# Optimization experiments

Hardware: AMD Instinct MI355X
Metric: run time of the kernel (lower is better)

## Reference

```python
import jax, jax.numpy as jnp
import numpy as np

DIM, BIN = 128, 16
LN_EPS = 1e-5


def setup_inputs() -> dict:
    key = jax.random.key(0)
    ks = jax.random.split(key, 16)
    B, Ld, Lc, O = 4096, 50, 50, 64
    D_VOCAB, C_VOCAB = 100000, 1000
    inp = {
        "discrete_index": jax.random.randint(ks[0], (B, Ld), 0, D_VOCAB, dtype=jnp.int32),
        "discrete_mask": jax.random.randint(ks[1], (B, Ld), 0, 2, dtype=jnp.int32),
        "continue_value": jax.random.normal(ks[2], (B, Lc), dtype=jnp.float32),
        "continue_index": jax.random.randint(ks[3], (B, Lc), 0, C_VOCAB, dtype=jnp.int32),
        "continue_mask": jax.random.randint(ks[4], (B, Lc), 0, 2, dtype=jnp.int32),
        # learned parameters (last row = padding idx, zeroed like torch padding_idx init semantics)
        "disc_emb": jax.random.normal(ks[5], (D_VOCAB + 1, DIM), dtype=jnp.float32).at[D_VOCAB].set(0.0),
        "v_emb": jax.random.normal(ks[6], (C_VOCAB + 1, BIN), dtype=jnp.float32).at[C_VOCAB].set(0.0),
        "b1_emb": jax.random.normal(ks[7], (C_VOCAB + 1, BIN), dtype=jnp.float32).at[C_VOCAB].set(0.0),
        "w_emb": jax.random.normal(ks[8], (C_VOCAB + 1, DIM * BIN), dtype=jnp.float32).at[C_VOCAB].set(0.0),
        "b2_emb": jax.random.normal(ks[9], (C_VOCAB + 1, DIM), dtype=jnp.float32).at[C_VOCAB].set(0.0),
        "ln_gamma": jnp.ones((BIN,), dtype=jnp.float32),
        "ln_beta": jnp.zeros((BIN,), dtype=jnp.float32),
        "transform_matrix": jax.random.normal(ks[10], (O, Ld + Lc), dtype=jnp.float32),
    }
    return inp


def reference(discrete_index, discrete_mask, continue_value, continue_index, continue_mask,
              disc_emb, v_emb, b1_emb, w_emb, b2_emb, ln_gamma, ln_beta, transform_matrix):
    B, Lc = continue_index.shape
    # embedding gathers
    discrete_part = disc_emb[discrete_index]            # [B, Ld, D]
    v = v_emb[continue_index]                           # [B, Lc, BIN]
    b1 = b1_emb[continue_index]                         # [B, Lc, BIN]
    w = w_emb[continue_index].reshape(B, Lc, BIN, DIM)  # [B, Lc, BIN, D]
    b2 = b2_emb[continue_index]                         # [B, Lc, D]
    # per-token mini-MLP: LayerNorm(bin) + ReLU + bmm with per-token weight
    h = continue_value[..., None] * v + b1              # [B, Lc, BIN]
    mu = jnp.mean(h, axis=-1, keepdims=True)
    var = jnp.mean((h - mu) ** 2, axis=-1, keepdims=True)
    hn = (h - mu) * jax.lax.rsqrt(var + LN_EPS) * ln_gamma + ln_beta
    a = jax.nn.relu(hn)
    continuous_part = jnp.einsum('blk,blkd->bld', a, w) + b2  # [B, Lc, D]
    parts = jnp.concatenate([discrete_part, continuous_part], axis=1)  # [B, L, D]
    out = jnp.einsum('ol,bld->bod', transform_matrix, parts)           # [B, O, D]
    # mask (no-grad path in original)
    mvec = jnp.concatenate([1 - discrete_mask, 1 - continue_mask], axis=1).astype(jnp.float32)  # [B, L]
    full_mask = (1.0 - jnp.sign(jnp.einsum('ol,bl->bo', transform_matrix, mvec))).astype(jnp.int32)  # [B, O]
    return out, full_mask
```

## Files before the change

### kernel.cpp

```cpp
#include <hip/hip_runtime.h>
#include <hip/hip_bf16.h>

#define NB 4096
#define LD_ 50
#define LC_ 50
#define LTOT 100
#define DIM 128
#define BIN 16
#define NO 64
#define KPAD 128
#define LP 136
#define LN_EPS 1e-5f

typedef __attribute__((ext_vector_type(8))) short bf16x8;
typedef __attribute__((ext_vector_type(4))) float f32x4;

__device__ __forceinline__ unsigned short f2bf(float f) {
    return __builtin_bit_cast(unsigned short, __float2bfloat16(f));
}

__global__ __launch_bounds__(256) void convT_kernel(const float* __restrict__ T,
                                                    unsigned short* __restrict__ Tbf) {
    int t = blockIdx.x * 256 + threadIdx.x;
    if (t < NO * KPAD) {
        int o = t >> 7, k = t & 127;
        float v = (k < LTOT) ? T[o * LTOT + k] : 0.f;
        Tbf[t] = f2bf(v);
    }
}

__global__ __launch_bounds__(256) void fused_embed_kernel(
    const int* __restrict__ dindex,
    const int* __restrict__ dmask,
    const float* __restrict__ cval,
    const int* __restrict__ cindex,
    const int* __restrict__ cmask,
    const float* __restrict__ disc_emb,
    const float* __restrict__ v_emb,
    const float* __restrict__ b1_emb,
    const float* __restrict__ w_emb,
    const float* __restrict__ b2_emb,
    const float* __restrict__ ln_gamma,
    const float* __restrict__ ln_beta,
    const float* __restrict__ T,
    const unsigned short* __restrict__ Tbf,
    float* __restrict__ out,
    float* __restrict__ outmask)
{
    __shared__ unsigned short PbfT[DIM * LP];
    __shared__ float a_lds[LC_ * 17];
    __shared__ float buf32[8 * DIM];
    __shared__ float mvec[LTOT];

    const int b   = blockIdx.x;
    const int tid = threadIdx.x;

    if (tid < LC_) {
        const int l = tid;
        const int ci = cindex[b * LC_ + l];
        const float cv = cval[b * LC_ + l];
        float h[BIN];
        {
            const float4* V4  = reinterpret_cast<const float4*>(v_emb  + (size_t)ci * BIN);
            const float4* B14 = reinterpret_cast<const float4*>(b1_emb + (size_t)ci * BIN);
            #pragma unroll
            for (int q = 0; q < 4; ++q) {
                float4 vv = V4[q], b1v = B14[q];
                h[q*4+0] = cv * vv.x + b1v.x;
                h[q*4+1] = cv * vv.y + b1v.y;
                h[q*4+2] = cv * vv.z + b1v.z;
                h[q*4+3] = cv * vv.w + b1v.w;
            }
        }
        float mu = 0.f;
        #pragma unroll
        for (int k = 0; k < BIN; ++k) mu += h[k];
        mu *= (1.f / BIN);
        float var = 0.f;
        #pragma unroll
        for (int k = 0; k < BIN; ++k) { float t = h[k] - mu; var += t * t; }
        var *= (1.f / BIN);
        const float rstd = rsqrtf(var + LN_EPS);
        #pragma unroll
        for (int k = 0; k < BIN; ++k) {
            float a = (h[k] - mu) * rstd * ln_gamma[k] + ln_beta[k];
            a_lds[l * 17 + k] = fmaxf(a, 0.f);
        }
    }

    if (tid < LTOT) {
        int m = (tid < LD_) ? dmask[b * LD_ + tid] : cmask[b * LC_ + (tid - LD_)];
        mvec[tid] = 1.0f - (float)m;
    }

    {
        const int d  = tid & 127;
        const int hh = tid >> 7;
        unsigned short* row = &PbfT[d * LP];
        if (hh == 0) {
            #pragma unroll
            for (int q = 0; q < 4; ++q)
                *reinterpret_cast<uint2*>(&row[100 + q * 4]) = make_uint2(0u, 0u);
        } else {
            #pragma unroll
            for (int q = 0; q < 3; ++q)
                *reinterpret_cast<uint2*>(&row[116 + q * 4]) = make_uint2(0u, 0u);
        }
    }

    {
        const int d  = tid & 127;
        const int hh = tid >> 7;
        for (int q = hh; q < 12; q += 2) {
            const int l0 = q * 4;
            float f[4];
            #pragma unroll
            for (int j = 0; j < 4; ++j) {
                int idx = dindex[b * LD_ + l0 + j];
                f[j] = disc_emb[(size_t)idx * DIM + d];
            }
            unsigned int lo = (unsigned)f2bf(f[0]) | ((unsigned)f2bf(f[1]) << 16);
            unsigned int hi = (unsigned)f2bf(f[2]) | ((unsigned)f2bf(f[3]) << 16);
            *reinterpret_cast<uint2*>(&PbfT[d * LP + l0]) = make_uint2(lo, hi);
        }
        if (hh == 0) {
            float f0 = disc_emb[(size_t)dindex[b * LD_ + 48] * DIM + d];
            float f1 = disc_emb[(size_t)dindex[b * LD_ + 49] * DIM + d];
            *reinterpret_cast<unsigned int*>(&PbfT[d * LP + 48]) =
                (unsigned)f2bf(f0) | ((unsigned)f2bf(f1) << 16);
        }
    }

    __syncthreads();

    if (tid < NO) {
        float s = 0.f;
        for (int l = 0; l < LTOT; ++l) s += T[tid * LTOT + l] * mvec[l];
        float sg = (s > 0.f) ? 1.f : ((s < 0.f) ? -1.f : 0.f);
        outmask[(size_t)b * NO + tid] = 1.f - sg;
    }

    const int dq = tid & 31;
    const int ts = tid >> 5;

    if (ts < 2) {
        const int lc = ts;
        const int ci = cindex[b * LC_ + lc];
        float4 acc = *reinterpret_cast<const float4*>(b2_emb + (size_t)ci * DIM + dq * 4);
        #pragma unroll
        for (int k = 0; k < BIN; ++k) {
            const float a = a_lds[lc * 17 + k];
            float4 w4 = *reinterpret_cast<const float4*>(w_emb + (size_t)ci * (BIN * DIM) + k * DIM + dq * 4);
            acc.x += a * w4.x; acc.y += a * w4.y; acc.z += a * w4.z; acc.w += a * w4.w;
        }
        *reinterpret_cast<float4*>(&buf32[ts * DIM + dq * 4]) = acc;
    }
    __syncthreads();
    if (tid < 128) {
        unsigned int v = (unsigned)f2bf(buf32[tid]) | ((unsigned)f2bf(buf32[DIM + tid]) << 16);
        *reinterpret_cast<unsigned int*>(&PbfT[tid * LP + 50]) = v;
    }
    __syncthreads();

    for (int p = 0; p < 6; ++p) {
        {
            const int lc = 2 + p * 8 + ts;
            const int ci = cindex[b * LC_ + lc];
            float4 acc = *reinterpret_cast<const float4*>(b2_emb + (size_t)ci * DIM + dq * 4);
            #pragma unroll
            for (int k = 0; k < BIN; ++k) {
                const float a = a_lds[lc * 17 + k];
                float4 w4 = *reinterpret_cast<const float4*>(w_emb + (size_t)ci * (BIN * DIM) + k * DIM + dq * 4);
                acc.x += a * w4.x; acc.y += a * w4.y; acc.z += a * w4.z; acc.w += a * w4.w;
            }
            *reinterpret_cast<float4*>(&buf32[ts * DIM + dq * 4]) = acc;
        }
        __syncthreads();
        {
            const int d  = tid & 127;
            const int hh = tid >> 7;
            const int l0 = 52 + p * 8 + 4 * hh;
            float g0 = buf32[(4*hh + 0) * DIM + d];
            float g1 = buf32[(4*hh + 1) * DIM + d];
            float g2 = buf32[(4*hh + 2) * DIM + d];
            float g3 = buf32[(4*hh + 3) * DIM + d];
            unsigned int lo = (unsigned)f2bf(g0) | ((unsigned)f2bf(g1) << 16);
            unsigned int hi = (unsigned)f2bf(g2) | ((unsigned)f2bf(g3) << 16);
            *reinterpret_cast<uint2*>(&PbfT[d * LP + l0]) = make_uint2(lo, hi);
        }
        __syncthreads();
    }

    {
        const int w    = tid >> 6;
        const int lane = tid & 63;
        const int r16  = lane & 15;
        const int g4   = lane >> 4;

        f32x4 acc[8];
        #pragma unroll
        for (int nt = 0; nt < 8; ++nt) acc[nt] = (f32x4){0.f, 0.f, 0.f, 0.f};

        bf16x8 afr[4];
        const unsigned short* Ta = Tbf + (16 * w + r16) * KPAD + g4 * 8;
        #pragma unroll
        for (int kc = 0; kc < 4; ++kc)
            afr[kc] = *reinterpret_cast<const bf16x8*>(Ta + kc * 32);

        #pragma unroll
        for (int nt = 0; nt < 8; ++nt) {
            const unsigned short* Bp = &PbfT[(nt * 16 + r16) * LP + g4 * 8];
            #pragma unroll
            for (int kc = 0; kc < 4; ++kc) {
                bf16x8 bfr = *reinterpret_cast<const bf16x8*>(Bp + kc * 32);
                acc[nt] = __builtin_amdgcn_mfma_f32_16x16x32_bf16(afr[kc], bfr, acc[nt], 0, 0, 0);
            }
        }

        float* ob = out + (size_t)b * NO * DIM + (size_t)(16 * w) * DIM;
        #pragma unroll
        for (int nt = 0; nt < 8; ++nt) {
            #pragma unroll
            for (int r = 0; r < 4; ++r) {
                ob[(g4 * 4 + r) * DIM + nt * 16 + r16] = acc[nt][r];
            }
        }
    }
}

extern "C" void kernel_launch(void* const* d_in, const int* in_sizes, int n_in,
                              void* d_out, int out_size, void* d_ws, size_t ws_size,
                              hipStream_t stream) {
    const int*   dindex  = (const int*)  d_in[0];
    const int*   dmask   = (const int*)  d_in[1];
    const float* cval    = (const float*)d_in[2];
    const int*   cindex  = (const int*)  d_in[3];
    const int*   cmask   = (const int*)  d_in[4];
    const float* disc_emb= (const float*)d_in[5];
    const float* v_emb   = (const float*)d_in[6];
    const float* b1_emb  = (const float*)d_in[7];
    const float* w_emb   = (const float*)d_in[8];
    const float* b2_emb  = (const float*)d_in[9];
    const float* lng     = (const float*)d_in[10];
    const float* lnb     = (const float*)d_in[11];
    const float* T       = (const float*)d_in[12];

    float* out     = (float*)d_out;
    float* outmask = out + (size_t)NB * NO * DIM;

    unsigned short* Tbf = (unsigned short*)d_ws;

    hipLaunchKernelGGL(convT_kernel, dim3((NO * KPAD + 255) / 256), dim3(256), 0, stream, T, Tbf);
    hipLaunchKernelGGL(fused_embed_kernel, dim3(NB), dim3(256), 0, stream,
                       dindex, dmask, cval, cindex, cmask,
                       disc_emb, v_emb, b1_emb, w_emb, b2_emb,
                       lng, lnb, T, Tbf, out, outmask);
}
```

Before: 376.7 us.

## Pre-convert w_emb to bf16 and compute continuous tokens per-wave without block barriers

Adds a pre-pass kernel that converts the per-token weight table w_emb to bf16 in the workspace, which halves the bytes gathered per continuous token. The LayerNorm mini-MLP is restructured so each wave handles two tokens, one per half-wave. The LN reduction uses shuffles and the activations are broadcast with __shfl, replacing the separate LDS staging phase and the six rounds of __syncthreads. This trades extra precision loss in the weights and an added conversion launch on every call for less gather traffic and fewer block-wide syncs.

After: 323.5 us. -14.1%, faster.

```diff
diff --git a/kernel.cpp b/kernel.cpp
--- a/kernel.cpp
+++ b/kernel.cpp
@@ -18,6 +18,18 @@
 __device__ __forceinline__ unsigned short f2bf(float f) {
     return __builtin_bit_cast(unsigned short, __float2bfloat16(f));
 }
+__device__ __forceinline__ float bf2f(unsigned u16) {
+    return __builtin_bit_cast(float, u16 << 16);
+}
+
+__global__ __launch_bounds__(256) void convW_kernel(const float* __restrict__ w,
+                                                    unsigned short* __restrict__ wbf) {
+    int t = blockIdx.x * 256 + threadIdx.x;
+    float4 v = *reinterpret_cast<const float4*>(w + (size_t)t * 4);
+    unsigned lo = (unsigned)f2bf(v.x) | ((unsigned)f2bf(v.y) << 16);
+    unsigned hi = (unsigned)f2bf(v.z) | ((unsigned)f2bf(v.w) << 16);
+    *reinterpret_cast<uint2*>(wbf + (size_t)t * 4) = make_uint2(lo, hi);
+}
 
 __global__ __launch_bounds__(256) void convT_kernel(const float* __restrict__ T,
                                                     unsigned short* __restrict__ Tbf) {
@@ -38,7 +50,7 @@
     const float* __restrict__ disc_emb,
     const float* __restrict__ v_emb,
     const float* __restrict__ b1_emb,
-    const float* __restrict__ w_emb,
+    const unsigned short* __restrict__ w_bf,
     const float* __restrict__ b2_emb,
     const float* __restrict__ ln_gamma,
     const float* __restrict__ ln_beta,
@@ -48,45 +60,13 @@
     float* __restrict__ outmask)
 {
     __shared__ unsigned short PbfT[DIM * LP];
-    __shared__ float a_lds[LC_ * 17];
-    __shared__ float buf32[8 * DIM];
+    __shared__ float buf32[4][2][DIM];
     __shared__ float mvec[LTOT];
 
-    const int b   = blockIdx.x;
-    const int tid = threadIdx.x;
-
-    if (tid < LC_) {
-        const int l = tid;
-        const int ci = cindex[b * LC_ + l];
-        const float cv = cval[b * LC_ + l];
-        float h[BIN];
-        {
-            const float4* V4  = reinterpret_cast<const float4*>(v_emb  + (size_t)ci * BIN);
-            const float4* B14 = reinterpret_cast<const float4*>(b1_emb + (size_t)ci * BIN);
-            #pragma unroll
-            for (int q = 0; q < 4; ++q) {
-                float4 vv = V4[q], b1v = B14[q];
-                h[q*4+0] = cv * vv.x + b1v.x;
-                h[q*4+1] = cv * vv.y + b1v.y;
-                h[q*4+2] = cv * vv.z + b1v.z;
-                h[q*4+3] = cv * vv.w + b1v.w;
-            }
-        }
-        float mu = 0.f;
-        #pragma unroll
-        for (int k = 0; k < BIN; ++k) mu += h[k];
-        mu *= (1.f / BIN);
-        float var = 0.f;
-        #pragma unroll
-        for (int k = 0; k < BIN; ++k) { float t = h[k] - mu; var += t * t; }
-        var *= (1.f / BIN);
-        const float rstd = rsqrtf(var + LN_EPS);
-        #pragma unroll
-        for (int k = 0; k < BIN; ++k) {
-            float a = (h[k] - mu) * rstd * ln_gamma[k] + ln_beta[k];
-            a_lds[l * 17 + k] = fmaxf(a, 0.f);
-        }
-    }
+    const int b    = blockIdx.x;
+    const int tid  = threadIdx.x;
+    const int wave = tid >> 6;
+    const int lane = tid & 63;
 
     if (tid < LTOT) {
         int m = (tid < LD_) ? dmask[b * LD_ + tid] : cmask[b * LC_ + (tid - LD_)];
@@ -119,8 +99,8 @@
                 int idx = dindex[b * LD_ + l0 + j];
                 f[j] = disc_emb[(size_t)idx * DIM + d];
             }
-            unsigned int lo = (unsigned)f2bf(f[0]) | ((unsigned)f2bf(f[1]) << 16);
-            unsigned int hi = (unsigned)f2bf(f[2]) | ((unsigned)f2bf(f[3]) << 16);
+            unsigned lo = (unsigned)f2bf(f[0]) | ((unsigned)f2bf(f[1]) << 16);
+            unsigned hi = (unsigned)f2bf(f[2]) | ((unsigned)f2bf(f[3]) << 16);
             *reinterpret_cast<uint2*>(&PbfT[d * LP + l0]) = make_uint2(lo, hi);
         }
         if (hh == 0) {
@@ -131,6 +111,62 @@
         }
     }
 
+    {
+        const int th = lane >> 5;
+        const int q  = lane & 31;
+        const int bcast = lane & 32;
+
+        for (int p = wave; p < 25; p += 4) {
+            const int t  = p * 2 + th;
+            const int ci = cindex[b * LC_ + t];
+            const float cv = cval[b * LC_ + t];
+
+            float a_val = 0.f;
+            if (q < 16) {
+                float h = cv * v_emb[ci * BIN + q] + b1_emb[ci * BIN + q];
+                float s = h;
+                s += __shfl_xor(s, 1, 16);
+                s += __shfl_xor(s, 2, 16);
+                s += __shfl_xor(s, 4, 16);
+                s += __shfl_xor(s, 8, 16);
+                float mu = s * (1.f / BIN);
+                float e  = h - mu;
+                float v2 = e * e;
+                v2 += __shfl_xor(v2, 1, 16);
+                v2 += __shfl_xor(v2, 2, 16);
+                v2 += __shfl_xor(v2, 4, 16);
+                v2 += __shfl_xor(v2, 8, 16);
+                float rstd = rsqrtf(v2 * (1.f / BIN) + LN_EPS);
+                a_val = fmaxf(e * rstd * ln_gamma[q] + ln_beta[q], 0.f);
+            }
+
+            float4 acc = *reinterpret_cast<const float4*>(b2_emb + (size_t)ci * DIM + q * 4);
+            const uint2* wp = reinterpret_cast<const uint2*>(w_bf + (size_t)ci * (BIN * DIM) + q * 4);
+            #pragma unroll
+            for (int k = 0; k < BIN; ++k) {
+                float ak = __shfl(a_val, bcast + k);
+                uint2 wv = wp[k * 32];
+                acc.x += ak * bf2f(wv.x & 0xffffu);
+                acc.y += ak * bf2f(wv.x >> 16);
+                acc.z += ak * bf2f(wv.y & 0xffffu);
+                acc.w += ak * bf2f(wv.y >> 16);
+            }
+
+            *reinterpret_cast<float4*>(&buf32[wave][th][q * 4]) = acc;
+            __builtin_amdgcn_wave_barrier();
+            float x0 = buf32[wave][0][lane];
+            float x1 = buf32[wave][1][lane];
+            float x2 = buf32[wave][0][lane + 64];
+            float x3 = buf32[wave][1][lane + 64];
+            __builtin_amdgcn_wave_barrier();
+            const int l0 = 50 + p * 2;
+            *reinterpret_cast<unsigned int*>(&PbfT[lane * LP + l0]) =
+                (unsigned)f2bf(x0) | ((unsigned)f2bf(x1) << 16);
+            *reinterpret_cast<unsigned int*>(&PbfT[(lane + 64) * LP + l0]) =
+                (unsigned)f2bf(x2) | ((unsigned)f2bf(x3) << 16);
+        }
+    }
+
     __syncthreads();
 
     if (tid < NO) {
@@ -140,69 +176,16 @@
         outmask[(size_t)b * NO + tid] = 1.f - sg;
     }
 
-    const int dq = tid & 31;
-    const int ts = tid >> 5;
-
-    if (ts < 2) {
-        const int lc = ts;
-        const int ci = cindex[b * LC_ + lc];
-        float4 acc = *reinterpret_cast<const float4*>(b2_emb + (size_t)ci * DIM + dq * 4);
-        #pragma unroll
-        for (int k = 0; k < BIN; ++k) {
-            const float a = a_lds[lc * 17 + k];
-            float4 w4 = *reinterpret_cast<const float4*>(w_emb + (size_t)ci * (BIN * DIM) + k * DIM + dq * 4);
-            acc.x += a * w4.x; acc.y += a * w4.y; acc.z += a * w4.z; acc.w += a * w4.w;
-        }
-        *reinterpret_cast<float4*>(&buf32[ts * DIM + dq * 4]) = acc;
-    }
-    __syncthreads();
-    if (tid < 128) {
-        unsigned int v = (unsigned)f2bf(buf32[tid]) | ((unsigned)f2bf(buf32[DIM + tid]) << 16);
-        *reinterpret_cast<unsigned int*>(&PbfT[tid * LP + 50]) = v;
-    }
-    __syncthreads();
-
-    for (int p = 0; p < 6; ++p) {
-        {
-            const int lc = 2 + p * 8 + ts;
-            const int ci = cindex[b * LC_ + lc];
-            float4 acc = *reinterpret_cast<const float4*>(b2_emb + (size_t)ci * DIM + dq * 4);
-            #pragma unroll
-            for (int k = 0; k < BIN; ++k) {
-                const float a = a_lds[lc * 17 + k];
-                float4 w4 = *reinterpret_cast<const float4*>(w_emb + (size_t)ci * (BIN * DIM) + k * DIM + dq * 4);
-                acc.x += a * w4.x; acc.y += a * w4.y; acc.z += a * w4.z; acc.w += a * w4.w;
-            }
-            *reinterpret_cast<float4*>(&buf32[ts * DIM + dq * 4]) = acc;
-        }
-        __syncthreads();
-        {
-            const int d  = tid & 127;
-            const int hh = tid >> 7;
-            const int l0 = 52 + p * 8 + 4 * hh;
-            float g0 = buf32[(4*hh + 0) * DIM + d];
-            float g1 = buf32[(4*hh + 1) * DIM + d];
-            float g2 = buf32[(4*hh + 2) * DIM + d];
-            float g3 = buf32[(4*hh + 3) * DIM + d];
-            unsigned int lo = (unsigned)f2bf(g0) | ((unsigned)f2bf(g1) << 16);
-            unsigned int hi = (unsigned)f2bf(g2) | ((unsigned)f2bf(g3) << 16);
-            *reinterpret_cast<uint2*>(&PbfT[d * LP + l0]) = make_uint2(lo, hi);
-        }
-        __syncthreads();
-    }
-
-    {
-        const int w    = tid >> 6;
-        const int lane = tid & 63;
-        const int r16  = lane & 15;
-        const int g4   = lane >> 4;
+    {
+        const int r16 = lane & 15;
+        const int g4  = lane >> 4;
 
         f32x4 acc[8];
         #pragma unroll
         for (int nt = 0; nt < 8; ++nt) acc[nt] = (f32x4){0.f, 0.f, 0.f, 0.f};
 
         bf16x8 afr[4];
-        const unsigned short* Ta = Tbf + (16 * w + r16) * KPAD + g4 * 8;
+        const unsigned short* Ta = Tbf + (16 * wave + r16) * KPAD + g4 * 8;
         #pragma unroll
         for (int kc = 0; kc < 4; ++kc)
             afr[kc] = *reinterpret_cast<const bf16x8*>(Ta + kc * 32);
@@ -217,7 +200,7 @@
             }
         }
 
-        float* ob = out + (size_t)b * NO * DIM + (size_t)(16 * w) * DIM;
+        float* ob = out + (size_t)b * NO * DIM + (size_t)(16 * wave) * DIM;
         #pragma unroll
         for (int nt = 0; nt < 8; ++nt) {
             #pragma unroll
@@ -248,11 +231,13 @@
     float* out     = (float*)d_out;
     float* outmask = out + (size_t)NB * NO * DIM;
 
-    unsigned short* Tbf = (unsigned short*)d_ws;
-
-    hipLaunchKernelGGL(convT_kernel, dim3((NO * KPAD + 255) / 256), dim3(256), 0, stream, T, Tbf);
+    unsigned short* w_bf = (unsigned short*)d_ws;
+    unsigned short* Tbf  = (unsigned short*)((char*)d_ws + 4100096);
+
+    hipLaunchKernelGGL(convW_kernel, dim3(2002), dim3(256), 0, stream, w_emb, w_bf);
+    hipLaunchKernelGGL(convT_kernel, dim3(32), dim3(256), 0, stream, T, Tbf);
     hipLaunchKernelGGL(fused_embed_kernel, dim3(NB), dim3(256), 0, stream,
                        dindex, dmask, cval, cindex, cmask,
-                       disc_emb, v_emb, b1_emb, w_emb, b2_emb,
+                       disc_emb, v_emb, b1_emb, w_bf, b2_emb,
                        lng, lnb, T, Tbf, out, outmask);
 }
```
